# Optimization experiments

Measured on AMD Instinct MI355X. Metric: run time of the kernel, lower is better.

The kernel has to match this reference:

```python
import jax, jax.numpy as jnp
import numpy as np

NEG = -1e30  # log-space 'zero' that stays finite in fp32
EPS = 1e-7   # keras backend epsilon used by ctc_batch_cost


def _lse3(a, b, c):
    m = jnp.maximum(jnp.maximum(a, b), c)
    return m + jnp.log(jnp.exp(a - m) + jnp.exp(b - m) + jnp.exp(c - m))


def setup_inputs() -> dict:
    key = jax.random.key(0)
    k1, k2 = jax.random.split(key)
    B, T, C, U = 256, 1024, 128, 128
    logits = jax.random.normal(k1, (B, T, C), dtype=jnp.float32)
    y_pred = jax.nn.softmax(logits, axis=-1)  # ctc_batch_cost expects probabilities
    y_true = jax.random.randint(k2, (B, U), 0, C - 1)  # labels in [0, C-2]; blank = C-1
    return {"y_true": y_true, "y_pred": y_pred}


def reference(y_true, y_pred):
    # Faithful to tf.keras.backend.ctc_batch_cost with input_length = T,
    # label_length = U for every row; blank index = num_classes - 1.
    B, T, C = y_pred.shape
    U = y_true.shape[1]
    S = 2 * U + 1
    blank = C - 1

    logp = jnp.log(y_pred + EPS)  # [B, T, C]

    # Extended label sequence: blank, l1, blank, l2, ..., lU, blank
    ext = jnp.full((B, S), blank, dtype=y_true.dtype).at[:, 1::2].set(y_true)

    # Per-timestep log-probs of extended labels: [B, T, S]
    lp_ext = jnp.take_along_axis(logp, jnp.broadcast_to(ext[:, None, :], (B, T, S)), axis=2)

    # Skip transition s-2 -> s allowed iff ext[s] != blank and ext[s] != ext[s-2]
    allow = jnp.concatenate(
        [jnp.zeros((B, 2), bool), (ext[:, 2:] != blank) & (ext[:, 2:] != ext[:, :-2])],
        axis=1,
    )  # [B, S]

    alpha0 = (
        jnp.full((B, S), NEG, dtype=logp.dtype)
        .at[:, 0].set(lp_ext[:, 0, 0])
        .at[:, 1].set(lp_ext[:, 0, 1])
    )

    lp_t = jnp.moveaxis(lp_ext, 1, 0)  # [T, B, S]

    def step(alpha, lp):
        a1 = jnp.concatenate([jnp.full((B, 1), NEG, alpha.dtype), alpha[:, :-1]], axis=1)
        a2 = jnp.concatenate([jnp.full((B, 2), NEG, alpha.dtype), alpha[:, :-2]], axis=1)
        a2 = jnp.where(allow, a2, NEG)
        alpha = _lse3(alpha, a1, a2) + lp
        return alpha, None

    alphaT, _ = jax.lax.scan(step, alpha0, lp_t[1:])

    a, b = alphaT[:, S - 1], alphaT[:, S - 2]
    m = jnp.maximum(a, b)
    ll = m + jnp.log(jnp.exp(a - m) + jnp.exp(b - m))
    return (-ll)[:, None]  # [B, 1], matching ctc_batch_cost
```

## Files before the change

kernel.cpp:

```cpp
#include <hip/hip_runtime.h>
#include <math.h>


#define T_DIM 1024
#define C_DIM 128
#define U_DIM 128
#define LN2F  0.6931471805599453f

#define EPS_LIT "0x33d6bf95"


#define RD(RC1,RC3,RCB,ROFF,RBOFF) \
  "ds_read_b32 " RC1 ", v12 offset:" ROFF "\n\t" \
  "ds_read_b32 " RC3 ", v13 offset:" ROFF "\n\t" \
  "ds_read_b32 " RCB ", v14 offset:" RBOFF "\n\t"

#define CMT(RC1,RC3,RCB) \
  "v_add_f32 v27, " EPS_LIT ", " RC1 "\n\t" \
  "v_add_f32 v28, " EPS_LIT ", " RC3 "\n\t" \
  "v_add_f32 v26, " EPS_LIT ", " RCB "\n\t"

#define ALPHA \
  "v_mov_b32_dpp v23, %[A3] wave_shr:1 row_mask:0xf bank_mask:0xf bound_ctrl:0\n\t" \
  "v_add_f32 v24, %[A0], v23\n\t" \
  "v_add_f32 v25, %[A0], %[A1]\n\t" \
  "v_fma_f32 v25, v23, v30, v25\n\t" \
  "v_mul_f32 %[A0], v24, v26\n\t" \
  "v_add_f32 v24, %[A1], %[A2]\n\t" \
  "v_add_f32 v23, %[A2], %[A3]\n\t" \
  "v_fma_f32 v23, %[A1], v31, v23\n\t" \
  "v_mul_f32 %[A1], v25, v27\n\t" \
  "v_mul_f32 %[A2], v24, v26\n\t" \
  "v_add_f32 v24, %[A3], %[A4]\n\t" \
  "v_mul_f32 %[A3], v23, v28\n\t" \
  "v_mul_f32 %[A4], v24, v26\n\t"

#define RENORM \
  "v_max_f32 v29, %[A0], %[A1]\n\t" \
  "v_max_f32 v29, v29, %[A2]\n\t" \
  "v_max_f32 v29, v29, %[A3]\n\t" \
  "v_max_f32 v29, v29, %[A4]\n\t" \
  "s_nop 1\n\t" \
  "v_max_f32_dpp v29, v29, v29 row_ror:8 row_mask:0xf bank_mask:0xf\n\t" \
  "s_nop 1\n\t" \
  "v_max_f32_dpp v29, v29, v29 row_ror:4 row_mask:0xf bank_mask:0xf\n\t" \
  "s_nop 1\n\t" \
  "v_max_f32_dpp v29, v29, v29 row_ror:2 row_mask:0xf bank_mask:0xf\n\t" \
  "s_nop 1\n\t" \
  "v_max_f32_dpp v29, v29, v29 row_ror:1 row_mask:0xf bank_mask:0xf\n\t" \
  "s_nop 1\n\t" \
  "v_readlane_b32 s91, v29, 0\n\t" \
  "v_readlane_b32 s92, v29, 16\n\t" \
  "v_readlane_b32 s93, v29, 32\n\t" \
  "v_readlane_b32 s94, v29, 48\n\t" \
  "s_nop 1\n\t" \
  "s_max_u32 s91, s91, s92\n\t" \
  "s_max_u32 s93, s93, s94\n\t" \
  "s_max_u32 s91, s91, s93\n\t" \
  "s_lshr_b32 s92, s91, 23\n\t" \
  "s_and_b32 s92, s92, 0xff\n\t" \
  "s_sub_u32 s93, 0x126, s92\n\t" \
  "s_min_u32 s93, s93, 0xfe\n\t" \
  "s_lshl_b32 s94, s93, 23\n\t" \
  "s_sub_u32 s95, 0x7f, s93\n\t" \
  "s_add_u32 %[EA], %[EA], s95\n\t" \
  "v_mul_f32 %[A0], s94, %[A0]\n\t" \
  "v_mul_f32 %[A1], s94, %[A1]\n\t" \
  "v_mul_f32 %[A2], s94, %[A2]\n\t" \
  "v_mul_f32 %[A3], s94, %[A3]\n\t" \
  "v_mul_f32 %[A4], s94, %[A4]\n\t"

#define SE(QW,WOFF,QL,RBOFF) \
  "s_waitcnt vmcnt(14)\n\t" \
  "ds_write_b128 v11, v[" QW "] offset:" WOFF "\n\t" \
  "global_load_dwordx4 v[" QL "], v10, %[P]\n\t" \
  "v_add_u32 v10, 0x400, v10\n\t" \
  "s_waitcnt lgkmcnt(4)\n\t" \
  CMT("v16","v17","v18") \
  RD("v16","v17","v18", WOFF, RBOFF) \
  ALPHA

#define SO(ROFF,RBOFF) \
  "s_waitcnt lgkmcnt(4)\n\t" \
  CMT("v19","v20","v21") \
  RD("v19","v20","v21", ROFF, RBOFF) \
  ALPHA

#define TE(VC,QW,WOFF,RBOFF) \
  "s_waitcnt vmcnt(" VC ")\n\t" \
  "ds_write_b128 v11, v[" QW "] offset:" WOFF "\n\t" \
  "s_waitcnt lgkmcnt(4)\n\t" \
  CMT("v16","v17","v18") \
  RD("v16","v17","v18", WOFF, RBOFF) \
  ALPHA

__global__ __launch_bounds__(64) void ctc_alpha_kernel(
    const int*   __restrict__ y_true,
    const float* __restrict__ y_pred,
    float*       __restrict__ out,
    int B)
{
  __shared__ float4 ldsbuf[1024];

  const int b = blockIdx.x;
  if (b >= B) return;
  const int lane = threadIdx.x;
  const float* __restrict__ p  = y_pred + (size_t)b * (T_DIM * C_DIM);
  const int*   __restrict__ yb = y_true + b * U_DIM;
  const int blank = C_DIM - 1;

  const int ylab0 = yb[2 * lane];
  const int ylab1 = yb[2 * lane + 1];
  int yprev = blank;
  if (lane > 0) yprev = yb[2 * lane - 1];
  const float allow1 = (lane > 0 && ylab0 != blank && ylab0 != yprev) ? 1.0f : 0.0f;
  const float allow3 = (ylab1 != blank && ylab1 != ylab0)             ? 1.0f : 0.0f;

  const unsigned lds_off = (unsigned)(uintptr_t)(void*)ldsbuf;
  const int gvoff = lane * 16;
  const int wraddr = (int)lds_off + lane * 16;
  const int rd1    = (int)lds_off + ylab0 * 4;
  const int rd3    = (int)lds_off + ylab1 * 4;
  const int rdb    = (int)lds_off;

  float a0 = (lane == 0) ? 1.0f : 0.0f;
  float a1 = 0.f, a2 = 0.f, a3 = 0.f, a4 = 0.f;
  int   e_acc = 0;

  asm volatile(
    "s_mov_b32 m0, -1\n\t"
    "v_mov_b32 v10, %[GV]\n\t"
    "v_mov_b32 v11, %[WA]\n\t"
    "v_mov_b32 v12, %[R1]\n\t"
    "v_mov_b32 v13, %[R3]\n\t"
    "v_mov_b32 v14, %[RB]\n\t"
    "v_mov_b32 v30, %[L1]\n\t"
    "v_mov_b32 v31, %[L3]\n\t"
    "global_load_dwordx4 v[32:35], v10, %[P]\n\t" "v_add_u32 v10, 0x400, v10\n\t"
    "global_load_dwordx4 v[36:39], v10, %[P]\n\t" "v_add_u32 v10, 0x400, v10\n\t"
    "global_load_dwordx4 v[40:43], v10, %[P]\n\t" "v_add_u32 v10, 0x400, v10\n\t"
    "global_load_dwordx4 v[44:47], v10, %[P]\n\t" "v_add_u32 v10, 0x400, v10\n\t"
    "global_load_dwordx4 v[48:51], v10, %[P]\n\t" "v_add_u32 v10, 0x400, v10\n\t"
    "global_load_dwordx4 v[52:55], v10, %[P]\n\t" "v_add_u32 v10, 0x400, v10\n\t"
    "global_load_dwordx4 v[56:59], v10, %[P]\n\t" "v_add_u32 v10, 0x400, v10\n\t"
    "global_load_dwordx4 v[60:63], v10, %[P]\n\t" "v_add_u32 v10, 0x400, v10\n\t"
    "global_load_dwordx4 v[64:67], v10, %[P]\n\t" "v_add_u32 v10, 0x400, v10\n\t"
    "global_load_dwordx4 v[68:71], v10, %[P]\n\t" "v_add_u32 v10, 0x400, v10\n\t"
    "global_load_dwordx4 v[72:75], v10, %[P]\n\t" "v_add_u32 v10, 0x400, v10\n\t"
    "global_load_dwordx4 v[76:79], v10, %[P]\n\t" "v_add_u32 v10, 0x400, v10\n\t"
    "global_load_dwordx4 v[80:83], v10, %[P]\n\t" "v_add_u32 v10, 0x400, v10\n\t"
    "global_load_dwordx4 v[84:87], v10, %[P]\n\t" "v_add_u32 v10, 0x400, v10\n\t"
    "global_load_dwordx4 v[88:91], v10, %[P]\n\t" "v_add_u32 v10, 0x400, v10\n\t"
    "global_load_dwordx4 v[92:95], v10, %[P]\n\t" "v_add_u32 v10, 0x400, v10\n\t"
    "s_waitcnt vmcnt(15)\n\t"
    "ds_write_b128 v11, v[32:35] offset:0\n\t"
    RD("v16","v17","v18", "0",   "508")
    RD("v19","v20","v21", "512", "1020")
    "s_mov_b32 s90, 31\n"
    "LM_%=:\n\t"
    SE("36:39","1024","32:35","1532")   SO("1536","2044")
    SE("40:43","2048","36:39","2556")   SO("2560","3068")
    SE("44:47","3072","40:43","3580")   SO("3584","4092")
    SE("48:51","4096","44:47","4604")   SO("4608","5116")   RENORM
    SE("52:55","5120","48:51","5628")   SO("5632","6140")
    SE("56:59","6144","52:55","6652")   SO("6656","7164")
    SE("60:63","7168","56:59","7676")   SO("7680","8188")
    SE("64:67","8192","60:63","8700")   SO("8704","9212")   RENORM
    SE("68:71","9216","64:67","9724")   SO("9728","10236")
    SE("72:75","10240","68:71","10748") SO("10752","11260")
    SE("76:79","11264","72:75","11772") SO("11776","12284")
    SE("80:83","12288","76:79","12796") SO("12800","13308") RENORM
    SE("84:87","13312","80:83","13820") SO("13824","14332")
    SE("88:91","14336","84:87","14844") SO("14848","15356")
    SE("92:95","15360","88:91","15868") SO("15872","16380")
    SE("32:35","0","92:95","508")       SO("512","1020")    RENORM
    "s_sub_u32 s90, s90, 1\n\t"
    "s_cmp_lg_u32 s90, 0\n\t"
    "s_cbranch_scc1 LM_%=\n\t"
    TE("14","36:39","1024","1532")   SO("1536","2044")
    TE("13","40:43","2048","2556")   SO("2560","3068")
    TE("12","44:47","3072","3580")   SO("3584","4092")
    TE("11","48:51","4096","4604")   SO("4608","5116")   RENORM
    TE("10","52:55","5120","5628")   SO("5632","6140")
    TE("9","56:59","6144","6652")    SO("6656","7164")
    TE("8","60:63","7168","7676")    SO("7680","8188")
    TE("7","64:67","8192","8700")    SO("8704","9212")   RENORM
    TE("6","68:71","9216","9724")    SO("9728","10236")
    TE("5","72:75","10240","10748")  SO("10752","11260")
    TE("4","76:79","11264","11772")  SO("11776","12284")
    TE("3","80:83","12288","12796")  SO("12800","13308") RENORM
    TE("2","84:87","13312","13820")  SO("13824","14332")
    TE("1","88:91","14336","14844")  SO("14848","15356")
    TE("0","92:95","15360","15868")  SO("15872","16380")
    "s_waitcnt lgkmcnt(3)\n\t"
    CMT("v16","v17","v18")
    ALPHA
    "s_waitcnt lgkmcnt(0)\n\t"
    CMT("v19","v20","v21")
    ALPHA
    RENORM
    : [A0]"+v"(a0), [A1]"+v"(a1), [A2]"+v"(a2), [A3]"+v"(a3), [A4]"+v"(a4),
      [EA]"+s"(e_acc)
    : [P]"s"(p), [GV]"v"(gvoff), [WA]"v"(wraddr), [R1]"v"(rd1), [R3]"v"(rd3),
      [RB]"v"(rdb), [L1]"v"(allow1), [L3]"v"(allow3)
    : "v10","v11","v12","v13","v14","v15","v16","v17","v18","v19","v20","v21",
      "v22","v23","v24","v25","v26","v27","v28","v29","v30","v31",
      "v32","v33","v34","v35","v36","v37","v38","v39","v40","v41","v42","v43",
      "v44","v45","v46","v47","v48","v49","v50","v51","v52","v53","v54","v55",
      "v56","v57","v58","v59","v60","v61","v62","v63","v64","v65","v66","v67",
      "v68","v69","v70","v71","v72","v73","v74","v75","v76","v77","v78","v79",
      "v80","v81","v82","v83","v84","v85","v86","v87","v88","v89","v90","v91",
      "v92","v93","v94","v95",
      "s90","s91","s92","s93","s94","s95","scc","memory");

  if (lane == 63) {
    float s = a3 + a4;
    s = fmaxf(s, 1e-37f);
    float ll = logf(s) + (float)e_acc * LN2F;
    out[b] = -ll;
  }
}

extern "C" void kernel_launch(void* const* d_in, const int* in_sizes, int n_in,
                              void* d_out, int out_size, void* d_ws, size_t ws_size,
                              hipStream_t stream) {
  const int*   y_true = (const int*)d_in[0];
  const float* y_pred = (const float*)d_in[1];
  float*       out    = (float*)d_out;
  const int B = in_sizes[0] / U_DIM;
  ctc_alpha_kernel<<<dim3(B), dim3(64), 0, stream>>>(y_true, y_pred, out, B);
}
```

Before: 202.4 us.

## Use packed FP32 math for alpha update and deepen LDS read pipeline

Rewrites the per-timestep alpha recurrence to use packed v_pk_add/v_pk_fma/v_pk_mul on register pairs, with the epsilon add for the gathered probabilities also done as a packed op. It moves the state into fixed registers. It deepens the software pipeline from two to four timesteps of LDS gathers in flight (lgkmcnt 11), using four rotating register sets, and issues the global prefetch one stage further ahead. The aim is to shorten the serial dependency chain per step and hide LDS latency. It adds register pressure and a few extra dummy reads and moves.

```diff
diff --git a/kernel.cpp b/kernel.cpp
--- a/kernel.cpp
+++ b/kernel.cpp
@@ -9,50 +9,45 @@
 
 #define EPS_LIT "0x33d6bf95"
 
-
-#define RD(RC1,RC3,RCB,ROFF,RBOFF) \
-  "ds_read_b32 " RC1 ", v12 offset:" ROFF "\n\t" \
-  "ds_read_b32 " RC3 ", v13 offset:" ROFF "\n\t" \
-  "ds_read_b32 " RCB ", v14 offset:" RBOFF "\n\t"
-
-#define CMT(RC1,RC3,RCB) \
-  "v_add_f32 v27, " EPS_LIT ", " RC1 "\n\t" \
-  "v_add_f32 v28, " EPS_LIT ", " RC3 "\n\t" \
-  "v_add_f32 v26, " EPS_LIT ", " RCB "\n\t"
+#define CMT(BP,BB) \
+  "v_add_f32 v120, v124, " BB "\n\t" \
+  "v_mov_b32 v121, v120\n\t" \
+  "v_pk_add_f32 v[122:123], " BP ", v[124:125]\n\t"
+
+#define RD(B0,B1,B2,ROFF,RBOFF) \
+  "ds_read_b32 " B0 ", v12 offset:" ROFF "\n\t" \
+  "ds_read_b32 " B1 ", v13 offset:" ROFF "\n\t" \
+  "ds_read_b32 " B2 ", v14 offset:" RBOFF "\n\t"
 
 #define ALPHA \
-  "v_mov_b32_dpp v23, %[A3] wave_shr:1 row_mask:0xf bank_mask:0xf bound_ctrl:0\n\t" \
-  "v_add_f32 v24, %[A0], v23\n\t" \
-  "v_add_f32 v25, %[A0], %[A1]\n\t" \
-  "v_fma_f32 v25, v23, v30, v25\n\t" \
-  "v_mul_f32 %[A0], v24, v26\n\t" \
-  "v_add_f32 v24, %[A1], %[A2]\n\t" \
-  "v_add_f32 v23, %[A2], %[A3]\n\t" \
-  "v_fma_f32 v23, %[A1], v31, v23\n\t" \
-  "v_mul_f32 %[A1], v25, v27\n\t" \
-  "v_mul_f32 %[A2], v24, v26\n\t" \
-  "v_add_f32 v24, %[A3], %[A4]\n\t" \
-  "v_mul_f32 %[A3], v23, v28\n\t" \
-  "v_mul_f32 %[A4], v24, v26\n\t"
+  "v_mov_b32_dpp v118, v115 wave_shr:1 row_mask:0xf bank_mask:0xf bound_ctrl:0\n\t" \
+  "v_mov_b32 v119, v114\n\t" \
+  "v_pk_add_f32 v[126:127], v[114:115], v[112:113]\n\t" \
+  "v_pk_fma_f32 v[126:127], v[118:119], v[30:31], v[126:127]\n\t" \
+  "v_pk_add_f32 v[112:113], v[112:113], v[118:119]\n\t" \
+  "v_add_f32 v117, v115, v116\n\t" \
+  "v_pk_mul_f32 v[114:115], v[126:127], v[122:123]\n\t" \
+  "v_pk_mul_f32 v[112:113], v[112:113], v[120:121]\n\t" \
+  "v_mul_f32 v116, v117, v120\n\t"
 
 #define RENORM \
-  "v_max_f32 v29, %[A0], %[A1]\n\t" \
-  "v_max_f32 v29, v29, %[A2]\n\t" \
-  "v_max_f32 v29, v29, %[A3]\n\t" \
-  "v_max_f32 v29, v29, %[A4]\n\t" \
-  "s_nop 1\n\t" \
-  "v_max_f32_dpp v29, v29, v29 row_ror:8 row_mask:0xf bank_mask:0xf\n\t" \
-  "s_nop 1\n\t" \
-  "v_max_f32_dpp v29, v29, v29 row_ror:4 row_mask:0xf bank_mask:0xf\n\t" \
-  "s_nop 1\n\t" \
-  "v_max_f32_dpp v29, v29, v29 row_ror:2 row_mask:0xf bank_mask:0xf\n\t" \
-  "s_nop 1\n\t" \
-  "v_max_f32_dpp v29, v29, v29 row_ror:1 row_mask:0xf bank_mask:0xf\n\t" \
-  "s_nop 1\n\t" \
-  "v_readlane_b32 s91, v29, 0\n\t" \
-  "v_readlane_b32 s92, v29, 16\n\t" \
-  "v_readlane_b32 s93, v29, 32\n\t" \
-  "v_readlane_b32 s94, v29, 48\n\t" \
+  "v_max_f32 v127, v112, v113\n\t" \
+  "v_max_f32 v127, v127, v114\n\t" \
+  "v_max_f32 v127, v127, v115\n\t" \
+  "v_max_f32 v127, v127, v116\n\t" \
+  "s_nop 1\n\t" \
+  "v_max_f32_dpp v127, v127, v127 row_ror:8 row_mask:0xf bank_mask:0xf\n\t" \
+  "s_nop 1\n\t" \
+  "v_max_f32_dpp v127, v127, v127 row_ror:4 row_mask:0xf bank_mask:0xf\n\t" \
+  "s_nop 1\n\t" \
+  "v_max_f32_dpp v127, v127, v127 row_ror:2 row_mask:0xf bank_mask:0xf\n\t" \
+  "s_nop 1\n\t" \
+  "v_max_f32_dpp v127, v127, v127 row_ror:1 row_mask:0xf bank_mask:0xf\n\t" \
+  "s_nop 1\n\t" \
+  "v_readlane_b32 s91, v127, 0\n\t" \
+  "v_readlane_b32 s92, v127, 16\n\t" \
+  "v_readlane_b32 s93, v127, 32\n\t" \
+  "v_readlane_b32 s94, v127, 48\n\t" \
   "s_nop 1\n\t" \
   "s_max_u32 s91, s91, s92\n\t" \
   "s_max_u32 s93, s93, s94\n\t" \
@@ -64,35 +59,42 @@
   "s_lshl_b32 s94, s93, 23\n\t" \
   "s_sub_u32 s95, 0x7f, s93\n\t" \
   "s_add_u32 %[EA], %[EA], s95\n\t" \
-  "v_mul_f32 %[A0], s94, %[A0]\n\t" \
-  "v_mul_f32 %[A1], s94, %[A1]\n\t" \
-  "v_mul_f32 %[A2], s94, %[A2]\n\t" \
-  "v_mul_f32 %[A3], s94, %[A3]\n\t" \
-  "v_mul_f32 %[A4], s94, %[A4]\n\t"
-
-#define SE(QW,WOFF,QL,RBOFF) \
-  "s_waitcnt vmcnt(14)\n\t" \
+  "v_mul_f32 v112, s94, v112\n\t" \
+  "v_mul_f32 v113, s94, v113\n\t" \
+  "v_mul_f32 v114, s94, v114\n\t" \
+  "v_mul_f32 v115, s94, v115\n\t" \
+  "v_mul_f32 v116, s94, v116\n\t"
+
+#define SE(...) SE_X(__VA_ARGS__)
+#define SO(...) SO_X(__VA_ARGS__)
+#define TE(...) TE_X(__VA_ARGS__)
+
+#define SE_X(QW,WOFF,QL,B0,B1,B2,BP,RBOFF) \
+  "s_waitcnt vmcnt(13)\n\t" \
   "ds_write_b128 v11, v[" QW "] offset:" WOFF "\n\t" \
   "global_load_dwordx4 v[" QL "], v10, %[P]\n\t" \
   "v_add_u32 v10, 0x400, v10\n\t" \
-  "s_waitcnt lgkmcnt(4)\n\t" \
-  CMT("v16","v17","v18") \
-  RD("v16","v17","v18", WOFF, RBOFF) \
-  ALPHA
-
-#define SO(ROFF,RBOFF) \
-  "s_waitcnt lgkmcnt(4)\n\t" \
-  CMT("v19","v20","v21") \
-  RD("v19","v20","v21", ROFF, RBOFF) \
-  ALPHA
-
-#define TE(VC,QW,WOFF,RBOFF) \
+  "s_waitcnt lgkmcnt(11)\n\t" \
+  CMT(BP,B2) RD(B0,B1,B2,WOFF,RBOFF) ALPHA
+
+#define SO_X(B0,B1,B2,BP,ROFF,RBOFF) \
+  "s_waitcnt lgkmcnt(11)\n\t" \
+  CMT(BP,B2) RD(B0,B1,B2,ROFF,RBOFF) ALPHA
+
+#define TE_X(VC,QW,WOFF,B0,B1,B2,BP,RBOFF) \
   "s_waitcnt vmcnt(" VC ")\n\t" \
   "ds_write_b128 v11, v[" QW "] offset:" WOFF "\n\t" \
-  "s_waitcnt lgkmcnt(4)\n\t" \
-  CMT("v16","v17","v18") \
-  RD("v16","v17","v18", WOFF, RBOFF) \
-  ALPHA
+  "s_waitcnt lgkmcnt(11)\n\t" \
+  CMT(BP,B2) RD(B0,B1,B2,WOFF,RBOFF) ALPHA
+
+#define FN(LGK,BP,BB) \
+  "s_waitcnt lgkmcnt(" LGK ")\n\t" \
+  CMT(BP,BB) ALPHA
+
+#define K0 "v96","v97","v98","v[96:97]"
+#define K1 "v100","v101","v102","v[100:101]"
+#define K2 "v104","v105","v106","v[104:105]"
+#define K3 "v108","v109","v110","v[108:109]"
 
 __global__ __launch_bounds__(64) void ctc_alpha_kernel(
     const int*   __restrict__ y_true,
@@ -123,8 +125,8 @@
   const int rd3    = (int)lds_off + ylab1 * 4;
   const int rdb    = (int)lds_off;
 
-  float a0 = (lane == 0) ? 1.0f : 0.0f;
-  float a1 = 0.f, a2 = 0.f, a3 = 0.f, a4 = 0.f;
+  const float init0 = (lane == 0) ? 1.0f : 0.0f;
+  float a3out, a4out;
   int   e_acc = 0;
 
   asm volatile(
@@ -136,6 +138,13 @@
     "v_mov_b32 v14, %[RB]\n\t"
     "v_mov_b32 v30, %[L1]\n\t"
     "v_mov_b32 v31, %[L3]\n\t"
+    "v_mov_b32 v112, %[I0]\n\t"
+    "v_mov_b32 v113, 0\n\t"
+    "v_mov_b32 v114, 0\n\t"
+    "v_mov_b32 v115, 0\n\t"
+    "v_mov_b32 v116, 0\n\t"
+    "v_mov_b32 v124, " EPS_LIT "\n\t"
+    "v_mov_b32 v125, " EPS_LIT "\n\t"
     "global_load_dwordx4 v[32:35], v10, %[P]\n\t" "v_add_u32 v10, 0x400, v10\n\t"
     "global_load_dwordx4 v[36:39], v10, %[P]\n\t" "v_add_u32 v10, 0x400, v10\n\t"
     "global_load_dwordx4 v[40:43], v10, %[P]\n\t" "v_add_u32 v10, 0x400, v10\n\t"
@@ -154,67 +163,81 @@
     "global_load_dwordx4 v[92:95], v10, %[P]\n\t" "v_add_u32 v10, 0x400, v10\n\t"
     "s_waitcnt vmcnt(15)\n\t"
     "ds_write_b128 v11, v[32:35] offset:0\n\t"
-    RD("v16","v17","v18", "0",   "508")
-    RD("v19","v20","v21", "512", "1020")
+    "s_waitcnt vmcnt(14)\n\t"
+    "ds_write_b128 v11, v[36:39] offset:1024\n\t"
+    "ds_read_b32 v96, v12 offset:0\n\t"
+    "ds_read_b32 v97, v13 offset:0\n\t"
+    "ds_read_b32 v98, v14 offset:508\n\t"
+    "ds_read_b32 v15, v14 offset:508\n\t"
+    "ds_read_b32 v100, v12 offset:512\n\t"
+    "ds_read_b32 v101, v13 offset:512\n\t"
+    "ds_read_b32 v102, v14 offset:1020\n\t"
+    "ds_read_b32 v15, v14 offset:508\n\t"
+    "ds_read_b32 v104, v12 offset:1024\n\t"
+    "ds_read_b32 v105, v13 offset:1024\n\t"
+    "ds_read_b32 v106, v14 offset:1532\n\t"
+    "ds_read_b32 v108, v12 offset:1536\n\t"
+    "ds_read_b32 v109, v13 offset:1536\n\t"
+    "ds_read_b32 v110, v14 offset:2044\n\t"
     "s_mov_b32 s90, 31\n"
     "LM_%=:\n\t"
-    SE("36:39","1024","32:35","1532")   SO("1536","2044")
-    SE("40:43","2048","36:39","2556")   SO("2560","3068")
-    SE("44:47","3072","40:43","3580")   SO("3584","4092")
-    SE("48:51","4096","44:47","4604")   SO("4608","5116")   RENORM
-    SE("52:55","5120","48:51","5628")   SO("5632","6140")
-    SE("56:59","6144","52:55","6652")   SO("6656","7164")
-    SE("60:63","7168","56:59","7676")   SO("7680","8188")
-    SE("64:67","8192","60:63","8700")   SO("8704","9212")   RENORM
-    SE("68:71","9216","64:67","9724")   SO("9728","10236")
-    SE("72:75","10240","68:71","10748") SO("10752","11260")
-    SE("76:79","11264","72:75","11772") SO("11776","12284")
-    SE("80:83","12288","76:79","12796") SO("12800","13308") RENORM
-    SE("84:87","13312","80:83","13820") SO("13824","14332")
-    SE("88:91","14336","84:87","14844") SO("14848","15356")
-    SE("92:95","15360","88:91","15868") SO("15872","16380")
-    SE("32:35","0","92:95","508")       SO("512","1020")    RENORM
+    SE("40:43","2048","32:35",K0,"2556")   SO(K1,"2560","3068")
+    SE("44:47","3072","36:39",K2,"3580")   SO(K3,"3584","4092")
+    SE("48:51","4096","40:43",K0,"4604")   SO(K1,"4608","5116")
+    SE("52:55","5120","44:47",K2,"5628")   SO(K3,"5632","6140")   RENORM
+    SE("56:59","6144","48:51",K0,"6652")   SO(K1,"6656","7164")
+    SE("60:63","7168","52:55",K2,"7676")   SO(K3,"7680","8188")
+    SE("64:67","8192","56:59",K0,"8700")   SO(K1,"8704","9212")
+    SE("68:71","9216","60:63",K2,"9724")   SO(K3,"9728","10236")  RENORM
+    SE("72:75","10240","64:67",K0,"10748") SO(K1,"10752","11260")
+    SE("76:79","11264","68:71",K2,"11772") SO(K3,"11776","12284")
+    SE("80:83","12288","72:75",K0,"12796") SO(K1,"12800","13308")
+    SE("84:87","13312","76:79",K2,"13820") SO(K3,"13824","14332") RENORM
+    SE("88:91","14336","80:83",K0,"14844") SO(K1,"14848","15356")
+    SE("92:95","15360","84:87",K2,"15868") SO(K3,"15872","16380")
+    SE("32:35","0","88:91",K0,"508")       SO(K1,"512","1020")
+    SE("36:39","1024","92:95",K2,"1532")   SO(K3,"1536","2044")   RENORM
     "s_sub_u32 s90, s90, 1\n\t"
     "s_cmp_lg_u32 s90, 0\n\t"
     "s_cbranch_scc1 LM_%=\n\t"
-    TE("14","36:39","1024","1532")   SO("1536","2044")
-    TE("13","40:43","2048","2556")   SO("2560","3068")
-    TE("12","44:47","3072","3580")   SO("3584","4092")
-    TE("11","48:51","4096","4604")   SO("4608","5116")   RENORM
-    TE("10","52:55","5120","5628")   SO("5632","6140")
-    TE("9","56:59","6144","6652")    SO("6656","7164")
-    TE("8","60:63","7168","7676")    SO("7680","8188")
-    TE("7","64:67","8192","8700")    SO("8704","9212")   RENORM
-    TE("6","68:71","9216","9724")    SO("9728","10236")
-    TE("5","72:75","10240","10748")  SO("10752","11260")
-    TE("4","76:79","11264","11772")  SO("11776","12284")
-    TE("3","80:83","12288","12796")  SO("12800","13308") RENORM
-    TE("2","84:87","13312","13820")  SO("13824","14332")
-    TE("1","88:91","14336","14844")  SO("14848","15356")
-    TE("0","92:95","15360","15868")  SO("15872","16380")
-    "s_waitcnt lgkmcnt(3)\n\t"
-    CMT("v16","v17","v18")
-    ALPHA
-    "s_waitcnt lgkmcnt(0)\n\t"
-    CMT("v19","v20","v21")
-    ALPHA
+    TE("13","40:43","2048",K0,"2556")   SO(K1,"2560","3068")
+    TE("12","44:47","3072",K2,"3580")   SO(K3,"3584","4092")
+    TE("11","48:51","4096",K0,"4604")   SO(K1,"4608","5116")
+    TE("10","52:55","5120",K2,"5628")   SO(K3,"5632","6140")   RENORM
+    TE("9","56:59","6144",K0,"6652")    SO(K1,"6656","7164")
+    TE("8","60:63","7168",K2,"7676")    SO(K3,"7680","8188")
+    TE("7","64:67","8192",K0,"8700")    SO(K1,"8704","9212")
+    TE("6","68:71","9216",K2,"9724")    SO(K3,"9728","10236")  RENORM
+    TE("5","72:75","10240",K0,"10748")  SO(K1,"10752","11260")
+    TE("4","76:79","11264",K2,"11772")  SO(K3,"11776","12284")
+    TE("3","80:83","12288",K0,"12796")  SO(K1,"12800","13308")
+    TE("2","84:87","13312",K2,"13820")  SO(K3,"13824","14332") RENORM
+    TE("1","88:91","14336",K0,"14844")  SO(K1,"14848","15356")
+    TE("0","92:95","15360",K2,"15868")  SO(K3,"15872","16380")
+    FN("10","v[96:97]","v98")
+    FN("7","v[100:101]","v102")
+    FN("3","v[104:105]","v106")
+    FN("0","v[108:109]","v110")
     RENORM
-    : [A0]"+v"(a0), [A1]"+v"(a1), [A2]"+v"(a2), [A3]"+v"(a3), [A4]"+v"(a4),
-      [EA]"+s"(e_acc)
+    "v_mov_b32 %[O3], v115\n\t"
+    "v_mov_b32 %[O4], v116\n\t"
+    : [O3]"=v"(a3out), [O4]"=v"(a4out), [EA]"+s"(e_acc)
     : [P]"s"(p), [GV]"v"(gvoff), [WA]"v"(wraddr), [R1]"v"(rd1), [R3]"v"(rd3),
-      [RB]"v"(rdb), [L1]"v"(allow1), [L3]"v"(allow3)
-    : "v10","v11","v12","v13","v14","v15","v16","v17","v18","v19","v20","v21",
-      "v22","v23","v24","v25","v26","v27","v28","v29","v30","v31",
+      [RB]"v"(rdb), [L1]"v"(allow1), [L3]"v"(allow3), [I0]"v"(init0)
+    : "v10","v11","v12","v13","v14","v15","v30","v31",
       "v32","v33","v34","v35","v36","v37","v38","v39","v40","v41","v42","v43",
       "v44","v45","v46","v47","v48","v49","v50","v51","v52","v53","v54","v55",
       "v56","v57","v58","v59","v60","v61","v62","v63","v64","v65","v66","v67",
       "v68","v69","v70","v71","v72","v73","v74","v75","v76","v77","v78","v79",
       "v80","v81","v82","v83","v84","v85","v86","v87","v88","v89","v90","v91",
-      "v92","v93","v94","v95",
+      "v92","v93","v94","v95","v96","v97","v98","v100","v101","v102",
+      "v104","v105","v106","v108","v109","v110","v112",
+      "v113","v114","v115","v116","v117","v118","v119","v120","v121","v122",
+      "v123","v124","v125","v126","v127",
       "s90","s91","s92","s93","s94","s95","scc","memory");
 
   if (lane == 63) {
-    float s = a3 + a4;
+    float s = a3out + a4out;
     s = fmaxf(s, 1e-37f);
     float ll = logf(s) + (float)e_acc * LN2F;
     out[b] = -ll;
```

After: 197.6 us. 1.02x faster.
